# Kernel tuning notes

Hardware: AMD Instinct MI355X
Metric: run time of the kernel (lower is better)

The kernel has to match this reference:

```python
import jax, jax.numpy as jnp
import numpy as np

B, S, D = 2, 2048, 2048
H = 16            # n_heads
DH = D // H       # d_head = 128
ROPE_BASE = 10000.0


def setup_inputs() -> dict:
    key = jax.random.key(0)
    ks = jax.random.split(key, 5)
    x = jax.random.normal(ks[0], (B, S, D), dtype=jnp.float32)
    s = 1.0 / np.sqrt(D).astype(np.float32)
    Wqkv = jax.random.normal(ks[1], (D, 3 * D), dtype=jnp.float32) * s
    bqkv = jnp.zeros((3 * D,), dtype=jnp.float32)
    Wo = jax.random.normal(ks[2], (D, D), dtype=jnp.float32) * s
    bo = jnp.zeros((D,), dtype=jnp.float32)
    return {"x": x, "Wqkv": Wqkv, "bqkv": bqkv, "Wo": Wo, "bo": bo}


def _rotary_tables(seq_len, d_head, dtype):
    inv_freq = 1.0 / (ROPE_BASE ** (jnp.arange(0, d_head, 2, dtype=dtype) / d_head))
    t = jnp.arange(seq_len, dtype=dtype)
    freqs = jnp.einsum('i,j->ij', t, inv_freq)          # [S, DH/2]
    emb = jnp.concatenate([freqs, freqs], axis=-1)       # [S, DH]
    return jnp.cos(emb), jnp.sin(emb)


def _rotate(u):
    # pairs (even, odd) -> cat(odd, -even) along last dim, per the source's
    # stack([::2],[1::2]) construction
    return jnp.concatenate([u[..., 1::2], -u[..., ::2]], axis=-1)


def reference(x, Wqkv, bqkv, Wo, bo):
    b, s, d = x.shape
    qkv = x @ Wqkv + bqkv                                # [B,S,3D]
    q, k, v = jnp.split(qkv, 3, axis=-1)
    # [B,S,D] -> [B,H,S,DH]
    q = q.reshape(b, s, H, DH).transpose(0, 2, 1, 3)
    k = k.reshape(b, s, H, DH).transpose(0, 2, 1, 3)
    v = v.reshape(b, s, H, DH).transpose(0, 2, 1, 3)
    cos, sin = _rotary_tables(s, DH, x.dtype)            # [S,DH], broadcasts over B,H
    q = q * cos + _rotate(q) * sin
    k = k * cos + _rotate(k) * sin
    scale = 1.0 / np.sqrt(DH).astype(np.float32)
    attn = jnp.einsum('bhqd,bhkd->bhqk', q, k) * scale   # [B,H,S,S]
    attn = jax.nn.softmax(attn, axis=-1)
    out = jnp.einsum('bhqk,bhkd->bhqd', attn, v)         # [B,H,S,DH]
    out = out.transpose(0, 2, 1, 3).reshape(b, s, d)
    return out @ Wo + bo
```

## Files before the change

kernel.cpp:

```cpp
#include <hip/hip_runtime.h>
#include <math.h>

constexpr int Bc = 2, Sc = 2048, Dc = 2048, Hc = 16, DHc = 128;
constexpr int Mc = Bc * Sc;
constexpr int N3 = 3 * Dc;

typedef short     s16x8  __attribute__((ext_vector_type(8)));
typedef float     f32x4  __attribute__((ext_vector_type(4)));
typedef unsigned short ushortv8 __attribute__((ext_vector_type(8)));

__device__ __forceinline__ unsigned short f2bf(float f) {
  unsigned u = __float_as_uint(f);
  u += 0x7fffu + ((u >> 16) & 1u);
  return (unsigned short)(u >> 16);
}
__device__ __forceinline__ float bf2f(unsigned short h) {
  return __uint_as_float(((unsigned)h) << 16);
}

__device__ __forceinline__ void gld_lds16(const unsigned short* g, unsigned short* l) {
  __builtin_amdgcn_global_load_lds(
      (const __attribute__((address_space(1))) void*)g,
      (__attribute__((address_space(3))) void*)l, 16, 0, 0);
}

template<int CTRL>
__device__ __forceinline__ float dppf(float x) {
  return __int_as_float(
      __builtin_amdgcn_update_dpp(0, __float_as_int(x), CTRL, 0xF, 0xF, true));
}
__device__ __forceinline__ float rowmax16(float v) {
  v = fmaxf(v, dppf<0xB1>(v));
  v = fmaxf(v, dppf<0x4E>(v));
  v = fmaxf(v, dppf<0x141>(v));
  v = fmaxf(v, dppf<0x140>(v));
  return v;
}
__device__ __forceinline__ float rowsum16(float v) {
  v += dppf<0xB1>(v);
  v += dppf<0x4E>(v);
  v += dppf<0x141>(v);
  v += dppf<0x140>(v);
  return v;
}

__global__ void rope_table_kernel(float* __restrict__ cosT, float* __restrict__ sinT) {
  int idx = blockIdx.x * 256 + threadIdx.x;
  int s = idx >> 6, j = idx & 63;
  float inv = powf(10000.0f, -(float)(2 * j) / 128.0f);
  float a = (float)s * inv;
  cosT[idx] = cosf(a);
  sinT[idx] = sinf(a);
}

__global__ void cvt_bf16(const float* __restrict__ in, unsigned short* __restrict__ outp) {
  size_t i = ((size_t)blockIdx.x * 256 + threadIdx.x) * 8;
  float4 a = *(const float4*)&in[i];
  float4 b = *(const float4*)&in[i + 4];
  ushortv8 o;
  o[0] = f2bf(a.x); o[1] = f2bf(a.y); o[2] = f2bf(a.z); o[3] = f2bf(a.w);
  o[4] = f2bf(b.x); o[5] = f2bf(b.y); o[6] = f2bf(b.z); o[7] = f2bf(b.w);
  *(ushortv8*)&outp[i] = o;
}

__global__ __launch_bounds__(256)
void cvt_transpose(const float* __restrict__ in, unsigned short* __restrict__ outp,
                   int R, int C) {
  __shared__ float Ls[64][69];
  const int nTc = C >> 6;
  const int tc = blockIdx.x % nTc, tr = blockIdx.x / nTc;
  const int r0 = tr << 6, c0 = tc << 6;
#pragma unroll
  for (int i = 0; i < 4; ++i) {
    int id = threadIdx.x + 256 * i;
    int row = id >> 4, col = (id & 15) << 2;
    float4 v = *(const float4*)&in[(size_t)(r0 + row) * C + c0 + col];
    Ls[row][col] = v.x; Ls[row][col + 1] = v.y;
    Ls[row][col + 2] = v.z; Ls[row][col + 3] = v.w;
  }
  __syncthreads();
#pragma unroll
  for (int i = 0; i < 2; ++i) {
    int id = threadIdx.x + 256 * i;
    int crow = id >> 3, rcol = (id & 7) << 3;
    ushortv8 o;
#pragma unroll
    for (int jj = 0; jj < 8; ++jj) o[jj] = f2bf(Ls[rcol + jj][crow]);
    *(ushortv8*)&outp[(size_t)(c0 + crow) * R + r0 + rcol] = o;
  }
}

template<int EPI>
__global__ __launch_bounds__(256)
void gemm_bt(const unsigned short* __restrict__ A, const unsigned short* __restrict__ Bt,
             const float* __restrict__ bias, unsigned short* __restrict__ Qo,
             unsigned short* __restrict__ Ko, unsigned short* __restrict__ Vo,
             float* __restrict__ outF, int Ndim)
{
  constexpr int Kd = 2048;
  __shared__ unsigned short As[128 * 32];
  __shared__ unsigned short Bs[128 * 32];
  const int t = threadIdx.x;
  const int w = t >> 6, l = t & 63;
  const int l15 = l & 15, g = l >> 4;
  const int wr = w >> 1, wc = w & 1;
  const int m0 = blockIdx.y * 128, n0 = blockIdx.x * 128;
  const int srow = l >> 2;
  const int scol = (l & 3) * 8;

  f32x4 acc[4][4];
#pragma unroll
  for (int mi = 0; mi < 4; ++mi)
#pragma unroll
    for (int ni = 0; ni < 4; ++ni) acc[mi][ni] = (f32x4){0.f, 0.f, 0.f, 0.f};

  for (int k0 = 0; k0 < Kd; k0 += 32) {
    __syncthreads();
#pragma unroll
    for (int j = 0; j < 2; ++j) {
      int rowg = (w * 2 + j) * 16 + srow;
      gld_lds16(&A[(size_t)(m0 + rowg) * Kd + k0 + scol], &As[(w * 2 + j) * 512]);
      gld_lds16(&Bt[(size_t)(n0 + rowg) * Kd + k0 + scol], &Bs[(w * 2 + j) * 512]);
    }
    __syncthreads();

    s16x8 af[4], bf[4];
#pragma unroll
    for (int mi = 0; mi < 4; ++mi)
      af[mi] = *(const s16x8*)&As[(wr * 64 + mi * 16 + l15) * 32 + g * 8];
#pragma unroll
    for (int ni = 0; ni < 4; ++ni)
      bf[ni] = *(const s16x8*)&Bs[(wc * 64 + ni * 16 + l15) * 32 + g * 8];
#pragma unroll
    for (int mi = 0; mi < 4; ++mi)
#pragma unroll
      for (int ni = 0; ni < 4; ++ni)
        acc[mi][ni] = __builtin_amdgcn_mfma_f32_16x16x32_bf16(af[mi], bf[ni], acc[mi][ni], 0, 0, 0);
  }

  if (EPI == 0) {
    const int part = n0 >> 11;
    const int h = (n0 >> 7) & 15;
    unsigned short* outp = (part == 0) ? Qo : (part == 1 ? Ko : Vo);
#pragma unroll
    for (int mi = 0; mi < 4; ++mi) {
#pragma unroll
      for (int r = 0; r < 4; ++r) {
        int row = m0 + wr * 64 + mi * 16 + g * 4 + r;
        int b_ = row >> 11, s_ = row & 2047;
        unsigned short* dst = outp + (((size_t)(b_ * Hc + h) * Sc + s_) << 7);
#pragma unroll
        for (int ni = 0; ni < 4; ++ni) {
          int col = wc * 64 + ni * 16 + l15;
          dst[col] = f2bf(acc[mi][ni][r] + bias[n0 + col]);
        }
      }
    }
  } else {
#pragma unroll
    for (int mi = 0; mi < 4; ++mi) {
#pragma unroll
      for (int r = 0; r < 4; ++r) {
        int row = m0 + wr * 64 + mi * 16 + g * 4 + r;
#pragma unroll
        for (int ni = 0; ni < 4; ++ni) {
          int col = wc * 64 + ni * 16 + l15;
          outF[(size_t)row * Ndim + n0 + col] = acc[mi][ni][r] + bias[n0 + col];
        }
      }
    }
  }
}

__global__ void rope_bf16(unsigned short* __restrict__ Q, unsigned short* __restrict__ K,
                          const float* __restrict__ cosT, const float* __restrict__ sinT) {
  const int row = blockIdx.x;
  const int t = threadIdx.x;
  const int half = t >> 7, j = t & 127;
  const int s = row & (Sc - 1);
  __shared__ float sh[2][128];
  unsigned short* buf = half ? K : Q;
  const size_t off = (size_t)row * DHc + j;
  float val = bf2f(buf[off]);
  sh[half][j] = val;
  __syncthreads();
  const float c  = cosT[s * 64 + (j & 63)];
  const float sn = sinT[s * 64 + (j & 63)];
  float rot = (j < 64) ? sh[half][2 * j + 1] : -sh[half][2 * (j - 64)];
  float r = val * c + rot * sn;
  if (!half) r *= 0.08838834764831845f;
  buf[off] = f2bf(r);
}

__global__ __launch_bounds__(256)
void vtrans(const unsigned short* __restrict__ V, unsigned short* __restrict__ Vt)
{
  __shared__ __align__(16) unsigned short Ls[64][132];
  const int bid = blockIdx.x;
  const int st = bid & 31, bh = bid >> 5;
  const int s0 = st * 64;
  const unsigned short* src = V + ((size_t)bh * Sc + s0) * DHc;
  unsigned short* dst = Vt + (size_t)bh * DHc * Sc + s0;
#pragma unroll
  for (int r = 0; r < 4; ++r) {
    int id = threadIdx.x + 256 * r;
    int row = id >> 4, col = (id & 15) * 8;
    *(ushortv8*)&Ls[row][col] = *(const ushortv8*)&src[(size_t)row * DHc + col];
  }
  __syncthreads();
#pragma unroll
  for (int r = 0; r < 4; ++r) {
    int id = threadIdx.x + 256 * r;
    int d = id >> 3, scol = (id & 7) * 8;
    ushortv8 o;
#pragma unroll
    for (int jj = 0; jj < 8; ++jj) o[jj] = Ls[scol + jj][d];
    *(ushortv8*)&dst[(size_t)d * Sc + scol] = o;
  }
}

__global__ __launch_bounds__(256)
void attn_mfma(const unsigned short* __restrict__ Qg, const unsigned short* __restrict__ Kg,
               const unsigned short* __restrict__ Vtg, unsigned short* __restrict__ Og)
{
  __shared__ __align__(16) unsigned short Ks[64][136];
  __shared__ __align__(16) unsigned short Vs[128][72];
  __shared__ __align__(16) unsigned short Ps[4][32][72];
  const int t = threadIdx.x;
  const int w = t >> 6, l = t & 63;
  const int l15 = l & 15, g = l >> 4;
  const int bid = blockIdx.x;
  const int qt = bid & 15, bh = bid >> 4;
  const int q0 = qt * 128;
  const size_t kbase = (size_t)bh * Sc * DHc;
  const size_t vbase = (size_t)bh * DHc * Sc;

  s16x8 qf[2][4];
#pragma unroll
  for (int mi = 0; mi < 2; ++mi)
#pragma unroll
    for (int ks = 0; ks < 4; ++ks)
      qf[mi][ks] = *(const s16x8*)&Qg[kbase + (size_t)(q0 + w * 32 + mi * 16 + l15) * DHc
                                      + ks * 32 + 8 * g];

  f32x4 acc[2][8];
#pragma unroll
  for (int mi = 0; mi < 2; ++mi)
#pragma unroll
    for (int dt = 0; dt < 8; ++dt) acc[mi][dt] = (f32x4){0.f, 0.f, 0.f, 0.f};
  float m_i[2][4], l_i[2][4];
#pragma unroll
  for (int mi = 0; mi < 2; ++mi)
#pragma unroll
    for (int r = 0; r < 4; ++r) { m_i[mi][r] = -1.0e30f; l_i[mi][r] = 0.f; }

  for (int kt0 = 0; kt0 < Sc; kt0 += 64) {
    __syncthreads();
#pragma unroll
    for (int r = 0; r < 4; ++r) {
      int id = t + 256 * r;
      int row = id >> 4, col = (id & 15) * 8;
      *(ushortv8*)&Ks[row][col] =
          *(const ushortv8*)&Kg[kbase + (size_t)(kt0 + row) * DHc + col];
    }
#pragma unroll
    for (int r = 0; r < 4; ++r) {
      int id = t + 256 * r;
      int row = id >> 3, col = (id & 7) * 8;
      *(ushortv8*)&Vs[row][col] =
          *(const ushortv8*)&Vtg[vbase + (size_t)row * Sc + kt0 + col];
    }
    __syncthreads();

    f32x4 sv[2][4];
#pragma unroll
    for (int mi = 0; mi < 2; ++mi)
#pragma unroll
      for (int nt = 0; nt < 4; ++nt) sv[mi][nt] = (f32x4){0.f, 0.f, 0.f, 0.f};
#pragma unroll
    for (int nt = 0; nt < 4; ++nt) {
#pragma unroll
      for (int ks = 0; ks < 4; ++ks) {
        s16x8 bf = *(const s16x8*)&Ks[nt * 16 + l15][ks * 32 + 8 * g];
        sv[0][nt] = __builtin_amdgcn_mfma_f32_16x16x32_bf16(qf[0][ks], bf, sv[0][nt], 0, 0, 0);
        sv[1][nt] = __builtin_amdgcn_mfma_f32_16x16x32_bf16(qf[1][ks], bf, sv[1][nt], 0, 0, 0);
      }
    }

#pragma unroll
    for (int mi = 0; mi < 2; ++mi) {
#pragma unroll
      for (int r = 0; r < 4; ++r) {
        float vmax = fmaxf(fmaxf(sv[mi][0][r], sv[mi][1][r]),
                           fmaxf(sv[mi][2][r], sv[mi][3][r]));
        vmax = rowmax16(vmax);
        float mnew = fmaxf(m_i[mi][r], vmax);
        float scf = __expf(m_i[mi][r] - mnew);
        float rs = 0.f;
#pragma unroll
        for (int nt = 0; nt < 4; ++nt) {
          float p = __expf(sv[mi][nt][r] - mnew);
          rs += p;
          Ps[w][mi * 16 + g * 4 + r][nt * 16 + l15] = f2bf(p);
        }
        rs = rowsum16(rs);
        l_i[mi][r] = l_i[mi][r] * scf + rs;
        m_i[mi][r] = mnew;
#pragma unroll
        for (int dt = 0; dt < 8; ++dt) acc[mi][dt][r] *= scf;
      }
    }

    s16x8 pf[2][2];
#pragma unroll
    for (int mi = 0; mi < 2; ++mi)
#pragma unroll
      for (int ks = 0; ks < 2; ++ks)
        pf[mi][ks] = *(const s16x8*)&Ps[w][mi * 16 + l15][ks * 32 + 8 * g];

#pragma unroll
    for (int dt = 0; dt < 8; ++dt) {
#pragma unroll
      for (int ks = 0; ks < 2; ++ks) {
        s16x8 vf = *(const s16x8*)&Vs[dt * 16 + l15][ks * 32 + 8 * g];
        acc[0][dt] = __builtin_amdgcn_mfma_f32_16x16x32_bf16(pf[0][ks], vf, acc[0][dt], 0, 0, 0);
        acc[1][dt] = __builtin_amdgcn_mfma_f32_16x16x32_bf16(pf[1][ks], vf, acc[1][dt], 0, 0, 0);
      }
    }
  }

  const int b = bh >> 4, h = bh & 15;
#pragma unroll
  for (int mi = 0; mi < 2; ++mi) {
#pragma unroll
    for (int r = 0; r < 4; ++r) {
      float inv = 1.0f / l_i[mi][r];
      int srow = q0 + w * 32 + mi * 16 + g * 4 + r;
      unsigned short* dst = Og + ((size_t)(b * Sc + srow)) * Dc + h * DHc;
#pragma unroll
      for (int dt = 0; dt < 8; ++dt)
        dst[dt * 16 + l15] = f2bf(acc[mi][dt][r] * inv);
    }
  }
}

extern "C" void kernel_launch(void* const* d_in, const int* in_sizes, int n_in,
                              void* d_out, int out_size, void* d_ws, size_t ws_size,
                              hipStream_t stream) {
  const float* x    = (const float*)d_in[0];
  const float* Wqkv = (const float*)d_in[1];
  const float* bqkv = (const float*)d_in[2];
  const float* Wo   = (const float*)d_in[3];
  const float* bo   = (const float*)d_in[4];
  float* out = (float*)d_out;
  char* p = (char*)d_ws;

  unsigned short* Ob  = (unsigned short*)p;  p += 16777216;
  float* cosT         = (float*)p;           p += 524288;
  float* sinT         = (float*)p;           p += 524288;
  unsigned short* xbf = (unsigned short*)p;  p += 16777216;
  unsigned short* Wqt = (unsigned short*)p;  p += 25165824;
  unsigned short* Wot = (unsigned short*)p;  p += 8388608;
  unsigned short* Qbf = (unsigned short*)p;  p += 16777216;
  unsigned short* Kbf = (unsigned short*)p;  p += 16777216;
  unsigned short* Vbf = (unsigned short*)p;  p += 16777216;
  unsigned short* Vtb = (unsigned short*)p;  p += 16777216;

  rope_table_kernel<<<(Sc * 64) / 256, 256, 0, stream>>>(cosT, sinT);

  cvt_bf16<<<(Mc * Dc) / (256 * 8), 256, 0, stream>>>(x, xbf);
  cvt_transpose<<<(N3 / 64) * (Dc / 64), 256, 0, stream>>>(Wqkv, Wqt, Dc, N3);
  cvt_transpose<<<(Dc / 64) * (Dc / 64), 256, 0, stream>>>(Wo, Wot, Dc, Dc);

  dim3 g1(N3 / 128, Mc / 128);
  gemm_bt<0><<<g1, 256, 0, stream>>>(xbf, Wqt, bqkv, Qbf, Kbf, Vbf, nullptr, N3);

  rope_bf16<<<Bc * Hc * Sc, 256, 0, stream>>>(Qbf, Kbf, cosT, sinT);

  vtrans<<<Bc * Hc * (Sc / 64), 256, 0, stream>>>(Vbf, Vtb);

  attn_mfma<<<Bc * Hc * (Sc / 128), 256, 0, stream>>>(Qbf, Kbf, Vtb, Ob);

  dim3 g2(Dc / 128, Mc / 128);
  gemm_bt<1><<<g2, 256, 0, stream>>>(Ob, Wot, bo, nullptr, nullptr, nullptr, out, Dc);
}
```

Baseline: 493.4 us.

## Swizzle workgroups, use exp2 softmax with lazy rescale, and raise MFMA priority

Remaps GEMM and attention workgroup IDs in an 8-way swizzle, which changes how tiles are spread across XCDs and caches. Folds log2(e) into the Q scale so the softmax can call exp2 directly. Skips the running-max update and accumulator rescale whenever the new row max stays within 8 of the old one, uniformly across the wave. Also changes the Ps LDS padding and wraps the MFMA loops in s_setprio. The lazy rescale lets unnormalized probabilities grow up to 2^8 before being corrected, which trades some numerical headroom for fewer rescale operations.

```diff
diff --git a/kernel.cpp b/kernel.cpp
--- a/kernel.cpp
+++ b/kernel.cpp
@@ -104,7 +104,10 @@
   const int w = t >> 6, l = t & 63;
   const int l15 = l & 15, g = l >> 4;
   const int wr = w >> 1, wc = w & 1;
-  const int m0 = blockIdx.y * 128, n0 = blockIdx.x * 128;
+  const int nwg = gridDim.x * gridDim.y;
+  const int flat = blockIdx.y * gridDim.x + blockIdx.x;
+  const int swz = (flat & 7) * (nwg >> 3) + (flat >> 3);
+  const int m0 = (swz / gridDim.x) * 128, n0 = (swz % gridDim.x) * 128;
   const int srow = l >> 2;
   const int scol = (l & 3) * 8;
 
@@ -188,7 +191,7 @@
   const float sn = sinT[s * 64 + (j & 63)];
   float rot = (j < 64) ? sh[half][2 * j + 1] : -sh[half][2 * (j - 64)];
   float r = val * c + rot * sn;
-  if (!half) r *= 0.08838834764831845f;
+  if (!half) r *= 0.08838834764831845f * 1.4426950408889634f;
   buf[off] = f2bf(r);
 }
 
@@ -225,12 +228,13 @@
 {
   __shared__ __align__(16) unsigned short Ks[64][136];
   __shared__ __align__(16) unsigned short Vs[128][72];
-  __shared__ __align__(16) unsigned short Ps[4][32][72];
+  __shared__ __align__(16) unsigned short Ps[4][32][68];
   const int t = threadIdx.x;
   const int w = t >> 6, l = t & 63;
   const int l15 = l & 15, g = l >> 4;
-  const int bid = blockIdx.x;
-  const int qt = bid & 15, bh = bid >> 4;
+  const int flat = blockIdx.x;
+  const int swz = (flat & 7) * 64 + (flat >> 3);
+  const int qt = swz & 15, bh = swz >> 4;
   const int q0 = qt * 128;
   const size_t kbase = (size_t)bh * Sc * DHc;
   const size_t vbase = (size_t)bh * DHc * Sc;
@@ -277,6 +281,7 @@
     for (int mi = 0; mi < 2; ++mi)
 #pragma unroll
       for (int nt = 0; nt < 4; ++nt) sv[mi][nt] = (f32x4){0.f, 0.f, 0.f, 0.f};
+    __builtin_amdgcn_s_setprio(1);
 #pragma unroll
     for (int nt = 0; nt < 4; ++nt) {
 #pragma unroll
@@ -286,28 +291,55 @@
         sv[1][nt] = __builtin_amdgcn_mfma_f32_16x16x32_bf16(qf[1][ks], bf, sv[1][nt], 0, 0, 0);
       }
     }
-
+    __builtin_amdgcn_s_setprio(0);
+
+    float vmax[2][4];
+    bool okb = true;
 #pragma unroll
     for (int mi = 0; mi < 2; ++mi) {
 #pragma unroll
       for (int r = 0; r < 4; ++r) {
-        float vmax = fmaxf(fmaxf(sv[mi][0][r], sv[mi][1][r]),
-                           fmaxf(sv[mi][2][r], sv[mi][3][r]));
-        vmax = rowmax16(vmax);
-        float mnew = fmaxf(m_i[mi][r], vmax);
-        float scf = __expf(m_i[mi][r] - mnew);
-        float rs = 0.f;
-#pragma unroll
-        for (int nt = 0; nt < 4; ++nt) {
-          float p = __expf(sv[mi][nt][r] - mnew);
-          rs += p;
-          Ps[w][mi * 16 + g * 4 + r][nt * 16 + l15] = f2bf(p);
+        float vm = fmaxf(fmaxf(sv[mi][0][r], sv[mi][1][r]),
+                         fmaxf(sv[mi][2][r], sv[mi][3][r]));
+        vm = rowmax16(vm);
+        vmax[mi][r] = vm;
+        okb = okb && (vm - m_i[mi][r] <= 8.0f);
+      }
+    }
+    if (__all((int)okb)) {
+#pragma unroll
+      for (int mi = 0; mi < 2; ++mi) {
+#pragma unroll
+        for (int r = 0; r < 4; ++r) {
+          float rs = 0.f;
+#pragma unroll
+          for (int nt = 0; nt < 4; ++nt) {
+            float p = __builtin_amdgcn_exp2f(sv[mi][nt][r] - m_i[mi][r]);
+            rs += p;
+            Ps[w][mi * 16 + g * 4 + r][nt * 16 + l15] = f2bf(p);
+          }
+          l_i[mi][r] += rowsum16(rs);
         }
-        rs = rowsum16(rs);
-        l_i[mi][r] = l_i[mi][r] * scf + rs;
-        m_i[mi][r] = mnew;
-#pragma unroll
-        for (int dt = 0; dt < 8; ++dt) acc[mi][dt][r] *= scf;
+      }
+    } else {
+#pragma unroll
+      for (int mi = 0; mi < 2; ++mi) {
+#pragma unroll
+        for (int r = 0; r < 4; ++r) {
+          float mnew = fmaxf(m_i[mi][r], vmax[mi][r]);
+          float scf = __builtin_amdgcn_exp2f(m_i[mi][r] - mnew);
+          float rs = 0.f;
+#pragma unroll
+          for (int nt = 0; nt < 4; ++nt) {
+            float p = __builtin_amdgcn_exp2f(sv[mi][nt][r] - mnew);
+            rs += p;
+            Ps[w][mi * 16 + g * 4 + r][nt * 16 + l15] = f2bf(p);
+          }
+          l_i[mi][r] = l_i[mi][r] * scf + rowsum16(rs);
+          m_i[mi][r] = mnew;
+#pragma unroll
+          for (int dt = 0; dt < 8; ++dt) acc[mi][dt][r] *= scf;
+        }
       }
     }
 
@@ -318,6 +350,7 @@
       for (int ks = 0; ks < 2; ++ks)
         pf[mi][ks] = *(const s16x8*)&Ps[w][mi * 16 + l15][ks * 32 + 8 * g];
 
+    __builtin_amdgcn_s_setprio(1);
 #pragma unroll
     for (int dt = 0; dt < 8; ++dt) {
 #pragma unroll
@@ -327,6 +360,7 @@
         acc[1][dt] = __builtin_amdgcn_mfma_f32_16x16x32_bf16(pf[1][ks], vf, acc[1][dt], 0, 0, 0);
       }
     }
+    __builtin_amdgcn_s_setprio(0);
   }
 
   const int b = bh >> 4, h = bh & 15;
```

Result: slower. 526.1 us (+6.6%).
